# Kernel tuning notes

Hardware: AMD Instinct MI355X
Metric: run time of the kernel (lower is better)

The kernel has to match this reference:

```python
import jax, jax.numpy as jnp
import numpy as np

H = 1024      # hidden_size
NH = 16       # num_heads
HD = H // NH  # head_dim


def setup_inputs() -> dict:
    key = jax.random.key(0)
    ks = jax.random.split(key, 5)
    x = jax.random.normal(ks[0], (2, 2048, H), dtype=jnp.float32)
    # nn.Linear weights are [out, in]; keep that convention
    w_qkv = jax.random.normal(ks[1], (3 * H, H), dtype=jnp.float32) * (1.0 / np.sqrt(H))
    b_qkv = jax.random.normal(ks[2], (3 * H,), dtype=jnp.float32) * 0.01
    w_out = jax.random.normal(ks[3], (H, H), dtype=jnp.float32) * (1.0 / np.sqrt(H))
    b_out = jax.random.normal(ks[4], (H,), dtype=jnp.float32) * 0.01
    return {"x": x, "w_qkv": w_qkv, "b_qkv": b_qkv, "w_out": w_out, "b_out": b_out}


def reference(x, w_qkv, b_qkv, w_out, b_out):
    B, L, _ = x.shape
    scale = HD ** -0.5
    qkv = x @ w_qkv.T + b_qkv                       # [B,L,3H]
    qkv = qkv.reshape(B, L, 3, NH, HD).transpose(2, 0, 3, 1, 4)  # [3,B,NH,L,HD]
    q, k, v = qkv[0], qkv[1], qkv[2]
    attn = jnp.einsum('bhqd,bhkd->bhqk', q, k) * scale
    attn = jax.nn.softmax(attn, axis=-1)            # dropout is identity in eval
    out = jnp.einsum('bhqk,bhkd->bhqd', attn, v)    # [B,NH,L,HD]
    out = out.transpose(0, 2, 1, 3).reshape(B, L, H)
    return out @ w_out.T + b_out
```

## Files before the change

kernel.cpp:

```cpp
#include <hip/hip_runtime.h>
#include <hip/hip_bf16.h>
#include <stdint.h>

#define H_DIM  1024
#define NHEADS 16
#define HDIM   64
#define BATCH  2
#define SEQ    2048
#define MROWS  (BATCH * SEQ)
#define QKV_N  (3 * H_DIM)
#define QK_LD  (2 * H_DIM)
#define NT     (SEQ / 64)

typedef __attribute__((ext_vector_type(8))) __bf16 bf16x8;
typedef __attribute__((ext_vector_type(4))) float  floatx4;

__device__ __forceinline__ unsigned short f2bf(float f) {
    uint32_t u = __float_as_uint(f);
    u += 0x7fffu + ((u >> 16) & 1u);
    return (unsigned short)(u >> 16);
}
__device__ __forceinline__ float bf2f(unsigned short u) {
    return __uint_as_float(((uint32_t)u) << 16);
}
__device__ __forceinline__ uint32_t cvtpk_bf16(float lo, float hi) {
    uint32_t r;
    asm("v_cvt_pk_bf16_f32 %0, %1, %2" : "=v"(r) : "v"(lo), "v"(hi));
    return r;
}

#if __has_builtin(__builtin_amdgcn_exp2f)
#define fexp2 __builtin_amdgcn_exp2f
#else
#define fexp2 exp2f
#endif

__device__ __forceinline__ void async_ld16(const void* g, void* l) {
    __builtin_amdgcn_global_load_lds(
        (const __attribute__((address_space(1))) void*)g,
        (__attribute__((address_space(3))) void*)l, 16, 0, 0);
}

#define N4_X   (MROWS * H_DIM / 4)
#define N4_WQ  (QKV_N * H_DIM / 4)
#define N4_WO  (H_DIM * H_DIM / 4)
__global__ __launch_bounds__(256) void cvt_all(const float4* __restrict__ x,
                                               const float4* __restrict__ wq,
                                               const float4* __restrict__ wo,
                                               ushort4* __restrict__ xb,
                                               ushort4* __restrict__ wqb,
                                               ushort4* __restrict__ wob) {
    int i = blockIdx.x * 256 + threadIdx.x;
    const float4* in;
    ushort4* out;
    int j;
    if (i < N4_X)                { in = x;  out = xb;  j = i; }
    else if (i < N4_X + N4_WQ)   { in = wq; out = wqb; j = i - N4_X; }
    else                         { in = wo; out = wob; j = i - N4_X - N4_WQ; }
    float4 v = in[j];
    ushort4 o;
    o.x = f2bf(v.x); o.y = f2bf(v.y); o.z = f2bf(v.z); o.w = f2bf(v.w);
    out[j] = o;
}

__global__ __launch_bounds__(256) void transpose_v(const unsigned short* __restrict__ vr,
                                                   unsigned short* __restrict__ vt) {
    __shared__ unsigned short T[64][72];
    const int tid = threadIdx.x;
    const int bh = blockIdx.y;
    const int b = bh >> 4, h = bh & 15;
    const int kv0 = blockIdx.x * 64;
    const int r  = tid >> 2, cs = (tid & 3) * 16;

    const unsigned short* src = &vr[(size_t)(b * SEQ + kv0 + r) * H_DIM + h * HDIM + cs];
    union { uint4 q; unsigned short u[8]; } A0, A1;
    A0.q = *(const uint4*)&src[0];
    A1.q = *(const uint4*)&src[8];
    #pragma unroll
    for (int e = 0; e < 8; ++e) T[cs + e][r]     = A0.u[e];
    #pragma unroll
    for (int e = 0; e < 8; ++e) T[cs + 8 + e][r] = A1.u[e];
    __syncthreads();

    const int dd = tid >> 2, ks = (tid & 3) * 16;
    unsigned short* dst = &vt[((size_t)bh * HDIM + dd) * SEQ + kv0 + ks];
    *(uint4*)&dst[0] = *(const uint4*)&T[dd][ks];
    *(uint4*)&dst[8] = *(const uint4*)&T[dd][ks + 8];
}

__global__ __launch_bounds__(256) void gemm_bt(const unsigned short* __restrict__ A,
                                               const unsigned short* __restrict__ B,
                                               const float* __restrict__ bias,
                                               unsigned short* __restrict__ Cb,
                                               float* __restrict__ Cf,
                                               unsigned short* __restrict__ Vr,
                                               int ldc, int Kdim) {
    __shared__ __align__(16) unsigned short As[128 * 64];
    __shared__ __align__(16) unsigned short Bs[128 * 64];
    const int tid  = threadIdx.x;
    const int lane = tid & 63;
    const int wave = tid >> 6;
    const int waveM = (wave >> 1) * 64;
    const int waveN = (wave & 1) * 64;

    const int nwg = gridDim.x * gridDim.y;
    int wg = blockIdx.y * gridDim.x + blockIdx.x;
    wg = (wg & 7) * (nwg >> 3) + (wg >> 3);
    const int bm = wg / gridDim.x, bn = wg % gridDim.x;

    floatx4 acc[4][4];
    #pragma unroll
    for (int i = 0; i < 4; ++i)
        #pragma unroll
        for (int j = 0; j < 4; ++j) {
            floatx4 z = {0.f, 0.f, 0.f, 0.f};
            acc[i][j] = z;
        }

    int rr[4], kc[4];
    #pragma unroll
    for (int i = 0; i < 4; ++i) {
        int c = i * 256 + tid;
        rr[i] = c >> 3;
        kc[i] = ((c & 7) ^ (rr[i] & 7)) * 8;
    }

    const int lr = lane & 15;
    const int g  = lane >> 4;
    const int sw = lr & 7;

    for (int k0 = 0; k0 < Kdim; k0 += 64) {
        #pragma unroll
        for (int i = 0; i < 4; ++i) {
            async_ld16(&A[(size_t)(bm * 128 + rr[i]) * Kdim + k0 + kc[i]],
                       (char*)As + i * 4096 + wave * 1024);
            async_ld16(&B[(size_t)(bn * 128 + rr[i]) * Kdim + k0 + kc[i]],
                       (char*)Bs + i * 4096 + wave * 1024);
        }
        __syncthreads();

        #pragma unroll
        for (int kk = 0; kk < 2; ++kk) {
            const int gk = (((kk << 2) + g) ^ sw) * 8;
            bf16x8 af[4], bfr[4];
            #pragma unroll
            for (int i = 0; i < 4; ++i)
                af[i] = *(const bf16x8*)&As[(waveM + i * 16 + lr) * 64 + gk];
            #pragma unroll
            for (int j = 0; j < 4; ++j)
                bfr[j] = *(const bf16x8*)&Bs[(waveN + j * 16 + lr) * 64 + gk];

            #pragma unroll
            for (int i = 0; i < 4; ++i)
                #pragma unroll
                for (int j = 0; j < 4; ++j)
                    acc[i][j] = __builtin_amdgcn_mfma_f32_16x16x32_bf16(af[i], bfr[j], acc[i][j], 0, 0, 0);
        }
        __syncthreads();
    }

    const int crow0 = bm * 128 + waveM + (lane >> 4) * 4;
    const int ccol0 = bn * 128 + waveN + (lane & 15);
    #pragma unroll
    for (int i = 0; i < 4; ++i)
        #pragma unroll
        for (int j = 0; j < 4; ++j) {
            int col = ccol0 + j * 16;
            float bv = bias[col];
            #pragma unroll
            for (int r = 0; r < 4; ++r) {
                int row = crow0 + i * 16 + r;
                float v = acc[i][j][r] + bv;
                if (Vr && col >= 2 * H_DIM) {
                    Vr[(size_t)row * H_DIM + (col - 2 * H_DIM)] = f2bf(v);
                } else if (Cb) {
                    Cb[(size_t)row * ldc + col] = f2bf(v);
                } else {
                    Cf[(size_t)row * ldc + col] = v;
                }
            }
        }
}

__global__ __launch_bounds__(256) void gemm_bt64(const unsigned short* __restrict__ A,
                                                 const unsigned short* __restrict__ B,
                                                 const float* __restrict__ bias,
                                                 float* __restrict__ Cf,
                                                 int ldc, int Kdim) {
    __shared__ __align__(16) unsigned short As[128 * 64];
    __shared__ __align__(16) unsigned short Bs[64 * 64];
    const int tid  = threadIdx.x;
    const int lane = tid & 63;
    const int wave = tid >> 6;
    const int waveM = wave * 32;

    const int nwg = gridDim.x * gridDim.y;
    int wg = blockIdx.y * gridDim.x + blockIdx.x;
    wg = (wg & 7) * (nwg >> 3) + (wg >> 3);
    const int bm = wg / gridDim.x, bn = wg % gridDim.x;

    floatx4 acc[2][4];
    #pragma unroll
    for (int i = 0; i < 2; ++i)
        #pragma unroll
        for (int j = 0; j < 4; ++j) {
            floatx4 z = {0.f, 0.f, 0.f, 0.f};
            acc[i][j] = z;
        }

    int rr[4], kc[4];
    #pragma unroll
    for (int i = 0; i < 4; ++i) {
        int c = i * 256 + tid;
        rr[i] = c >> 3;
        kc[i] = ((c & 7) ^ (rr[i] & 7)) * 8;
    }

    const int lr = lane & 15;
    const int g  = lane >> 4;
    const int sw = lr & 7;

    for (int k0 = 0; k0 < Kdim; k0 += 64) {
        #pragma unroll
        for (int i = 0; i < 4; ++i)
            async_ld16(&A[(size_t)(bm * 128 + rr[i]) * Kdim + k0 + kc[i]],
                       (char*)As + i * 4096 + wave * 1024);
        #pragma unroll
        for (int i = 0; i < 2; ++i)
            async_ld16(&B[(size_t)(bn * 64 + rr[i]) * Kdim + k0 + kc[i]],
                       (char*)Bs + i * 4096 + wave * 1024);
        __syncthreads();

        #pragma unroll
        for (int kk = 0; kk < 2; ++kk) {
            const int gk = (((kk << 2) + g) ^ sw) * 8;
            bf16x8 af[2], bfr[4];
            #pragma unroll
            for (int i = 0; i < 2; ++i)
                af[i] = *(const bf16x8*)&As[(waveM + i * 16 + lr) * 64 + gk];
            #pragma unroll
            for (int j = 0; j < 4; ++j)
                bfr[j] = *(const bf16x8*)&Bs[(j * 16 + lr) * 64 + gk];

            #pragma unroll
            for (int i = 0; i < 2; ++i)
                #pragma unroll
                for (int j = 0; j < 4; ++j)
                    acc[i][j] = __builtin_amdgcn_mfma_f32_16x16x32_bf16(af[i], bfr[j], acc[i][j], 0, 0, 0);
        }
        __syncthreads();
    }

    const int crow0 = bm * 128 + waveM + (lane >> 4) * 4;
    const int ccol0 = bn * 64 + (lane & 15);
    #pragma unroll
    for (int i = 0; i < 2; ++i)
        #pragma unroll
        for (int j = 0; j < 4; ++j) {
            int col = ccol0 + j * 16;
            float bv = bias[col];
            #pragma unroll
            for (int r = 0; r < 4; ++r) {
                int row = crow0 + i * 16 + r;
                Cf[(size_t)row * ldc + col] = acc[i][j][r] + bv;
            }
        }
}

__global__ __launch_bounds__(256, 4) void attn_mfma(const unsigned short* __restrict__ qkv2,
                                                    const unsigned short* __restrict__ vt,
                                                    unsigned short* __restrict__ ctx) {
    __shared__ __align__(16) unsigned short Ks2[2][64 * 64];
    __shared__ __align__(16) unsigned short Vt2[2][64 * 64];

    const int tid  = threadIdx.x;
    const int lane = tid & 63;
    const int wave = tid >> 6;
    const int bh = blockIdx.y;
    const int b  = bh >> 4, h = bh & 15;
    const int q0 = blockIdx.x * 64 + wave * 16;
    const int lq = lane & 15;
    const int g  = lane >> 4;
    const int swz = lq & 7;

    const float QS = 0.125f * 1.44269504f;
    bf16x8 qf[2];
    #pragma unroll
    for (int kk = 0; kk < 2; ++kk) {
        union { bf16x8 v; unsigned short u[8]; } tq;
        tq.v = *(const bf16x8*)&qkv2[(size_t)(b * SEQ + q0 + lq) * QK_LD
                                     + h * HDIM + kk * 32 + g * 8];
        #pragma unroll
        for (int e = 0; e < 8; ++e) tq.u[e] = f2bf(bf2f(tq.u[e]) * QS);
        qf[kk] = tq.v;
    }

    floatx4 acc_o[4];
    #pragma unroll
    for (int j = 0; j < 4; ++j) {
        floatx4 z = {0.f, 0.f, 0.f, 0.f};
        acc_o[j] = z;
    }
    float l_run = 0.f;

    const unsigned short* gK = qkv2 + (size_t)b * SEQ * QK_LD + H_DIM + (size_t)h * HDIM;
    const unsigned short* gV = vt + (size_t)bh * HDIM * SEQ;

    const int r0  = tid >> 3;
    const int pr0 = (r0 & 32) | ((r0 & 12) << 1) | ((r0 & 16) >> 2) | (r0 & 3);
    const int gs0 = (tid & 7) ^ (r0 & 7);
    const unsigned short* pK0 = gK + (size_t)pr0 * QK_LD + gs0 * 8;
    const unsigned short* pK1 = gK + (size_t)(pr0 + 32) * QK_LD + gs0 * 8;
    const unsigned short* pV0 = gV + (size_t)r0 * SEQ + gs0 * 8;
    const unsigned short* pV1 = gV + (size_t)(r0 + 32) * SEQ + gs0 * 8;

    #define STAGE_KV(bi)                                                        \
        {                                                                       \
            async_ld16(pK0, (char*)&Ks2[bi][0] + (wave * 64) * 16);             \
            async_ld16(pK1, (char*)&Ks2[bi][0] + (256 + wave * 64) * 16);       \
            async_ld16(pV0, (char*)&Vt2[bi][0] + (wave * 64) * 16);             \
            async_ld16(pV1, (char*)&Vt2[bi][0] + (256 + wave * 64) * 16);       \
            pK0 += 64 * QK_LD; pK1 += 64 * QK_LD; pV0 += 64; pV1 += 64;         \
        }

    STAGE_KV(0)
    __syncthreads();

    int buf = 0;
    for (int t = 0; t < NT; ++t) {
        if (t + 1 < NT) STAGE_KV(buf ^ 1)

        const unsigned short* Ksb = &Ks2[buf][0];
        const unsigned short* Vsb = &Vt2[buf][0];

        bf16x8 kf[4][2];
        #pragma unroll
        for (int jb = 0; jb < 4; ++jb)
            #pragma unroll
            for (int kk = 0; kk < 2; ++kk)
                kf[jb][kk] = *(const bf16x8*)&Ksb[(jb * 16 + lq) * 64 + (((kk << 2) + g) ^ swz) * 8];

        bf16x8 vf[4][2];
        #pragma unroll
        for (int dt = 0; dt < 4; ++dt)
            #pragma unroll
            for (int kk = 0; kk < 2; ++kk)
                vf[dt][kk] = *(const bf16x8*)&Vsb[(dt * 16 + lq) * 64 + (((kk << 2) + g) ^ swz) * 8];

        __builtin_amdgcn_sched_barrier(0);

        floatx4 sa[4];
        #pragma unroll
        for (int jb = 0; jb < 4; ++jb) {
            floatx4 z = {0.f, 0.f, 0.f, 0.f};
            sa[jb] = z;
        }
        __builtin_amdgcn_s_setprio(1);
        #pragma unroll
        for (int jb = 0; jb < 4; ++jb)
            #pragma unroll
            for (int kk = 0; kk < 2; ++kk)
                sa[jb] = __builtin_amdgcn_mfma_f32_16x16x32_bf16(kf[jb][kk], qf[kk], sa[jb], 0, 0, 0);
        __builtin_amdgcn_s_setprio(0);

        float ps = 0.f;

        {
            float e00 = fexp2(sa[0][0]), e01 = fexp2(sa[0][1]), e02 = fexp2(sa[0][2]), e03 = fexp2(sa[0][3]);
            float e10 = fexp2(sa[1][0]), e11 = fexp2(sa[1][1]), e12 = fexp2(sa[1][2]), e13 = fexp2(sa[1][3]);
            ps += ((e00 + e01) + (e02 + e03)) + ((e10 + e11) + (e12 + e13));
            union { bf16x8 v; uint32_t u[4]; } pf;
            pf.u[0] = cvtpk_bf16(e00, e01); pf.u[1] = cvtpk_bf16(e02, e03);
            pf.u[2] = cvtpk_bf16(e10, e11); pf.u[3] = cvtpk_bf16(e12, e13);
            __builtin_amdgcn_s_setprio(1);
            #pragma unroll
            for (int dt = 0; dt < 4; ++dt)
                acc_o[dt] = __builtin_amdgcn_mfma_f32_16x16x32_bf16(pf.v, vf[dt][0], acc_o[dt], 0, 0, 0);
            __builtin_amdgcn_s_setprio(0);
        }

        {
            float e00 = fexp2(sa[2][0]), e01 = fexp2(sa[2][1]), e02 = fexp2(sa[2][2]), e03 = fexp2(sa[2][3]);
            float e10 = fexp2(sa[3][0]), e11 = fexp2(sa[3][1]), e12 = fexp2(sa[3][2]), e13 = fexp2(sa[3][3]);
            ps += ((e00 + e01) + (e02 + e03)) + ((e10 + e11) + (e12 + e13));
            union { bf16x8 v; uint32_t u[4]; } pf;
            pf.u[0] = cvtpk_bf16(e00, e01); pf.u[1] = cvtpk_bf16(e02, e03);
            pf.u[2] = cvtpk_bf16(e10, e11); pf.u[3] = cvtpk_bf16(e12, e13);
            __builtin_amdgcn_s_setprio(1);
            #pragma unroll
            for (int dt = 0; dt < 4; ++dt)
                acc_o[dt] = __builtin_amdgcn_mfma_f32_16x16x32_bf16(pf.v, vf[dt][1], acc_o[dt], 0, 0, 0);
            __builtin_amdgcn_s_setprio(0);
        }

        ps += __shfl_xor(ps, 16);
        ps += __shfl_xor(ps, 32);
        l_run += ps;

        __syncthreads();
        buf ^= 1;
    }
    #undef STAGE_KV

    float linv[4];
    #pragma unroll
    for (int r = 0; r < 4; ++r)
        linv[r] = 1.f / __shfl(l_run, g * 4 + r);
    #pragma unroll
    for (int dt = 0; dt < 4; ++dt)
        #pragma unroll
        for (int r = 0; r < 4; ++r)
            ctx[(size_t)(b * SEQ + q0 + g * 4 + r) * H_DIM + h * HDIM + dt * 16 + lq]
                = f2bf(acc_o[dt][r] * linv[r]);
}

extern "C" void kernel_launch(void* const* d_in, const int* in_sizes, int n_in,
                              void* d_out, int out_size, void* d_ws, size_t ws_size,
                              hipStream_t stream) {
    const float* x     = (const float*)d_in[0];
    const float* w_qkv = (const float*)d_in[1];
    const float* b_qkv = (const float*)d_in[2];
    const float* w_out = (const float*)d_in[3];
    const float* b_out = (const float*)d_in[4];
    float* out = (float*)d_out;

    unsigned short* xb    = (unsigned short*)d_ws;
    unsigned short* wqkvb = xb    + (size_t)MROWS * H_DIM;
    unsigned short* woutb = wqkvb + (size_t)QKV_N * H_DIM;
    unsigned short* qkv2  = woutb + (size_t)H_DIM * H_DIM;
    unsigned short* ctxb  = qkv2  + (size_t)MROWS * QK_LD;
    unsigned short* vtb   = ctxb  + (size_t)MROWS * H_DIM;
    unsigned short* vrows = ctxb;

    cvt_all<<<(N4_X + N4_WQ + N4_WO) / 256, 256, 0, stream>>>(
        (const float4*)x, (const float4*)w_qkv, (const float4*)w_out,
        (ushort4*)xb, (ushort4*)wqkvb, (ushort4*)woutb);

    gemm_bt<<<dim3(QKV_N / 128, MROWS / 128), 256, 0, stream>>>(xb, wqkvb, b_qkv, qkv2, nullptr, vrows, QK_LD, H_DIM);

    transpose_v<<<dim3(SEQ / 64, BATCH * NHEADS), 256, 0, stream>>>(vrows, vtb);

    attn_mfma<<<dim3(SEQ / 64, BATCH * NHEADS), 256, 0, stream>>>(qkv2, vtb, ctxb);

    gemm_bt64<<<dim3(H_DIM / 64, MROWS / 128), 256, 0, stream>>>(ctxb, woutb, b_out, out, H_DIM, H_DIM);
}
```

Measured before the change: 189.7 us.

## Process 32 queries per wave in attention and swizzle block-to-head mapping

```diff
diff --git a/kernel.cpp b/kernel.cpp
--- a/kernel.cpp
+++ b/kernel.cpp
@@ -267,7 +267,7 @@
         }
 }
 
-__global__ __launch_bounds__(256, 4) void attn_mfma(const unsigned short* __restrict__ qkv2,
+__global__ __launch_bounds__(256, 2) void attn_mfma(const unsigned short* __restrict__ qkv2,
                                                     const unsigned short* __restrict__ vt,
                                                     unsigned short* __restrict__ ctx) {
     __shared__ __align__(16) unsigned short Ks2[2][64 * 64];
@@ -276,32 +276,39 @@
     const int tid  = threadIdx.x;
     const int lane = tid & 63;
     const int wave = tid >> 6;
-    const int bh = blockIdx.y;
+
+    const int f  = blockIdx.y * gridDim.x + blockIdx.x;
+    const int bh = ((f >> 7) << 3) + (f & 7);
+    const int qt = (f >> 3) & 15;
     const int b  = bh >> 4, h = bh & 15;
-    const int q0 = blockIdx.x * 64 + wave * 16;
+    const int q0 = qt * 128 + wave * 32;
     const int lq = lane & 15;
     const int g  = lane >> 4;
     const int swz = lq & 7;
 
     const float QS = 0.125f * 1.44269504f;
-    bf16x8 qf[2];
-    #pragma unroll
-    for (int kk = 0; kk < 2; ++kk) {
-        union { bf16x8 v; unsigned short u[8]; } tq;
-        tq.v = *(const bf16x8*)&qkv2[(size_t)(b * SEQ + q0 + lq) * QK_LD
-                                     + h * HDIM + kk * 32 + g * 8];
-        #pragma unroll
-        for (int e = 0; e < 8; ++e) tq.u[e] = f2bf(bf2f(tq.u[e]) * QS);
-        qf[kk] = tq.v;
-    }
-
-    floatx4 acc_o[4];
-    #pragma unroll
-    for (int j = 0; j < 4; ++j) {
-        floatx4 z = {0.f, 0.f, 0.f, 0.f};
-        acc_o[j] = z;
-    }
-    float l_run = 0.f;
+    bf16x8 qf[2][2];
+    #pragma unroll
+    for (int s = 0; s < 2; ++s)
+        #pragma unroll
+        for (int kk = 0; kk < 2; ++kk) {
+            union { bf16x8 v; unsigned short u[8]; } tq;
+            tq.v = *(const bf16x8*)&qkv2[(size_t)(b * SEQ + q0 + s * 16 + lq) * QK_LD
+                                         + h * HDIM + kk * 32 + g * 8];
+            #pragma unroll
+            for (int e = 0; e < 8; ++e) tq.u[e] = f2bf(bf2f(tq.u[e]) * QS);
+            qf[s][kk] = tq.v;
+        }
+
+    floatx4 acc_o[2][4];
+    #pragma unroll
+    for (int s = 0; s < 2; ++s)
+        #pragma unroll
+        for (int j = 0; j < 4; ++j) {
+            floatx4 z = {0.f, 0.f, 0.f, 0.f};
+            acc_o[s][j] = z;
+        }
+    float l_run[2] = {0.f, 0.f};
 
     const unsigned short* gK = qkv2 + (size_t)b * SEQ * QK_LD + H_DIM + (size_t)h * HDIM;
     const unsigned short* gV = vt + (size_t)bh * HDIM * SEQ;
@@ -349,69 +356,76 @@
 
         __builtin_amdgcn_sched_barrier(0);
 
-        floatx4 sa[4];
-        #pragma unroll
-        for (int jb = 0; jb < 4; ++jb) {
-            floatx4 z = {0.f, 0.f, 0.f, 0.f};
-            sa[jb] = z;
-        }
+        floatx4 sa[2][4];
+        #pragma unroll
+        for (int s = 0; s < 2; ++s)
+            #pragma unroll
+            for (int jb = 0; jb < 4; ++jb) {
+                floatx4 z = {0.f, 0.f, 0.f, 0.f};
+                sa[s][jb] = z;
+            }
         __builtin_amdgcn_s_setprio(1);
         #pragma unroll
-        for (int jb = 0; jb < 4; ++jb)
-            #pragma unroll
-            for (int kk = 0; kk < 2; ++kk)
-                sa[jb] = __builtin_amdgcn_mfma_f32_16x16x32_bf16(kf[jb][kk], qf[kk], sa[jb], 0, 0, 0);
+        for (int s = 0; s < 2; ++s)
+            #pragma unroll
+            for (int jb = 0; jb < 4; ++jb)
+                #pragma unroll
+                for (int kk = 0; kk < 2; ++kk)
+                    sa[s][jb] = __builtin_amdgcn_mfma_f32_16x16x32_bf16(kf[jb][kk], qf[s][kk], sa[s][jb], 0, 0, 0);
         __builtin_amdgcn_s_setprio(0);
 
-        float ps = 0.f;
-
-        {
-            float e00 = fexp2(sa[0][0]), e01 = fexp2(sa[0][1]), e02 = fexp2(sa[0][2]), e03 = fexp2(sa[0][3]);
-            float e10 = fexp2(sa[1][0]), e11 = fexp2(sa[1][1]), e12 = fexp2(sa[1][2]), e13 = fexp2(sa[1][3]);
-            ps += ((e00 + e01) + (e02 + e03)) + ((e10 + e11) + (e12 + e13));
-            union { bf16x8 v; uint32_t u[4]; } pf;
-            pf.u[0] = cvtpk_bf16(e00, e01); pf.u[1] = cvtpk_bf16(e02, e03);
-            pf.u[2] = cvtpk_bf16(e10, e11); pf.u[3] = cvtpk_bf16(e12, e13);
-            __builtin_amdgcn_s_setprio(1);
-            #pragma unroll
-            for (int dt = 0; dt < 4; ++dt)
-                acc_o[dt] = __builtin_amdgcn_mfma_f32_16x16x32_bf16(pf.v, vf[dt][0], acc_o[dt], 0, 0, 0);
-            __builtin_amdgcn_s_setprio(0);
-        }
-
-        {
-            float e00 = fexp2(sa[2][0]), e01 = fexp2(sa[2][1]), e02 = fexp2(sa[2][2]), e03 = fexp2(sa[2][3]);
-            float e10 = fexp2(sa[3][0]), e11 = fexp2(sa[3][1]), e12 = fexp2(sa[3][2]), e13 = fexp2(sa[3][3]);
-            ps += ((e00 + e01) + (e02 + e03)) + ((e10 + e11) + (e12 + e13));
-            union { bf16x8 v; uint32_t u[4]; } pf;
-            pf.u[0] = cvtpk_bf16(e00, e01); pf.u[1] = cvtpk_bf16(e02, e03);
-            pf.u[2] = cvtpk_bf16(e10, e11); pf.u[3] = cvtpk_bf16(e12, e13);
-            __builtin_amdgcn_s_setprio(1);
-            #pragma unroll
-            for (int dt = 0; dt < 4; ++dt)
-                acc_o[dt] = __builtin_amdgcn_mfma_f32_16x16x32_bf16(pf.v, vf[dt][1], acc_o[dt], 0, 0, 0);
-            __builtin_amdgcn_s_setprio(0);
-        }
-
-        ps += __shfl_xor(ps, 16);
-        ps += __shfl_xor(ps, 32);
-        l_run += ps;
+        #pragma unroll
+        for (int s = 0; s < 2; ++s) {
+            float ps = 0.f;
+            {
+                float e00 = fexp2(sa[s][0][0]), e01 = fexp2(sa[s][0][1]), e02 = fexp2(sa[s][0][2]), e03 = fexp2(sa[s][0][3]);
+                float e10 = fexp2(sa[s][1][0]), e11 = fexp2(sa[s][1][1]), e12 = fexp2(sa[s][1][2]), e13 = fexp2(sa[s][1][3]);
+                ps += ((e00 + e01) + (e02 + e03)) + ((e10 + e11) + (e12 + e13));
+                union { bf16x8 v; uint32_t u[4]; } pf;
+                pf.u[0] = cvtpk_bf16(e00, e01); pf.u[1] = cvtpk_bf16(e02, e03);
+                pf.u[2] = cvtpk_bf16(e10, e11); pf.u[3] = cvtpk_bf16(e12, e13);
+                __builtin_amdgcn_s_setprio(1);
+                #pragma unroll
+                for (int dt = 0; dt < 4; ++dt)
+                    acc_o[s][dt] = __builtin_amdgcn_mfma_f32_16x16x32_bf16(pf.v, vf[dt][0], acc_o[s][dt], 0, 0, 0);
+                __builtin_amdgcn_s_setprio(0);
+            }
+            {
+                float e00 = fexp2(sa[s][2][0]), e01 = fexp2(sa[s][2][1]), e02 = fexp2(sa[s][2][2]), e03 = fexp2(sa[s][2][3]);
+                float e10 = fexp2(sa[s][3][0]), e11 = fexp2(sa[s][3][1]), e12 = fexp2(sa[s][3][2]), e13 = fexp2(sa[s][3][3]);
+                ps += ((e00 + e01) + (e02 + e03)) + ((e10 + e11) + (e12 + e13));
+                union { bf16x8 v; uint32_t u[4]; } pf;
+                pf.u[0] = cvtpk_bf16(e00, e01); pf.u[1] = cvtpk_bf16(e02, e03);
+                pf.u[2] = cvtpk_bf16(e10, e11); pf.u[3] = cvtpk_bf16(e12, e13);
+                __builtin_amdgcn_s_setprio(1);
+                #pragma unroll
+                for (int dt = 0; dt < 4; ++dt)
+                    acc_o[s][dt] = __builtin_amdgcn_mfma_f32_16x16x32_bf16(pf.v, vf[dt][1], acc_o[s][dt], 0, 0, 0);
+                __builtin_amdgcn_s_setprio(0);
+            }
+            ps += __shfl_xor(ps, 16);
+            ps += __shfl_xor(ps, 32);
+            l_run[s] += ps;
+        }
 
         __syncthreads();
         buf ^= 1;
     }
     #undef STAGE_KV
 
-    float linv[4];
-    #pragma unroll
-    for (int r = 0; r < 4; ++r)
-        linv[r] = 1.f / __shfl(l_run, g * 4 + r);
-    #pragma unroll
-    for (int dt = 0; dt < 4; ++dt)
+    #pragma unroll
+    for (int s = 0; s < 2; ++s) {
+        float linv[4];
         #pragma unroll
         for (int r = 0; r < 4; ++r)
-            ctx[(size_t)(b * SEQ + q0 + g * 4 + r) * H_DIM + h * HDIM + dt * 16 + lq]
-                = f2bf(acc_o[dt][r] * linv[r]);
+            linv[r] = 1.f / __shfl(l_run[s], g * 4 + r);
+        #pragma unroll
+        for (int dt = 0; dt < 4; ++dt)
+            #pragma unroll
+            for (int r = 0; r < 4; ++r)
+                ctx[(size_t)(b * SEQ + q0 + s * 16 + g * 4 + r) * H_DIM + h * HDIM + dt * 16 + lq]
+                    = f2bf(acc_o[s][dt][r] * linv[r]);
+    }
 }
 
 extern "C" void kernel_launch(void* const* d_in, const int* in_sizes, int n_in,
@@ -440,7 +454,7 @@
 
     transpose_v<<<dim3(SEQ / 64, BATCH * NHEADS), 256, 0, stream>>>(vrows, vtb);
 
-    attn_mfma<<<dim3(SEQ / 64, BATCH * NHEADS), 256, 0, stream>>>(qkv2, vtb, ctxb);
+    attn_mfma<<<dim3(SEQ / 128, BATCH * NHEADS), 256, 0, stream>>>(qkv2, vtb, ctxb);
 
     gemm_bt64<<<dim3(H_DIM / 64, MROWS / 128), 256, 0, stream>>>(ctxb, woutb, b_out, out, H_DIM, H_DIM);
 }
```

Result: no change. 187.5 us (-1.2%).
